# Performance work log

Measured on AMD Instinct MI355X. Metric: run time of the kernel, lower is better.

## Reference

```python
import jax, jax.numpy as jnp
import numpy as np

SEQ_LEN = 4096
EMBED_DIM = 1280
NUM_HEADS = 16
HEAD_DIM = EMBED_DIM // NUM_HEADS  # 80
SCALING = float(np.sqrt(HEAD_DIM))  # NOTE: source multiplies by sqrt(head_dim)
NEG_INF = float(np.finfo(np.float32).min)


def rotate_half(x):
    x1, x2 = jnp.split(x, 2, axis=-1)
    return jnp.concatenate((-x2, x1), axis=-1)


def setup_inputs() -> dict:
    key = jax.random.key(0)
    ks = jax.random.split(key, 7)
    s = 0.02
    hidden_states = jax.random.normal(ks[0], (SEQ_LEN, EMBED_DIM), dtype=jnp.float32)
    w_qkv = jax.random.normal(ks[1], (3 * EMBED_DIM, EMBED_DIM), dtype=jnp.float32) * s
    b_qkv = jax.random.normal(ks[2], (3 * EMBED_DIM,), dtype=jnp.float32) * s
    w_proj = jax.random.normal(ks[3], (EMBED_DIM, EMBED_DIM), dtype=jnp.float32) * s
    b_proj = jax.random.normal(ks[4], (EMBED_DIM,), dtype=jnp.float32) * s
    # rotary angles: theta duplicated to head_dim (emb = cat(rope, rope))
    inv_freq = 1.0 / (10000.0 ** (jnp.arange(0, HEAD_DIM // 2, dtype=jnp.float32) * 2.0 / HEAD_DIM))
    pos = jnp.arange(SEQ_LEN, dtype=jnp.float32)
    freqs = pos[:, None] * inv_freq[None, :]            # [S, hd/2]
    emb = jnp.concatenate((freqs, freqs), axis=-1)       # [S, hd]
    cos = jnp.cos(emb)
    sin = jnp.sin(emb)
    # 4 packed images of 1024 patches each
    cu_seqlens = jnp.array([0, 1024, 2048, 3072, 4096], dtype=jnp.int32)
    return {
        "hidden_states": hidden_states,
        "w_qkv": w_qkv, "b_qkv": b_qkv,
        "w_proj": w_proj, "b_proj": b_proj,
        "cos": cos, "sin": sin,
        "cu_seqlens": cu_seqlens,
    }


def reference(hidden_states, w_qkv, b_qkv, w_proj, b_proj, cos, sin, cu_seqlens):
    S = hidden_states.shape[0]
    # packed QKV projection
    qkv = hidden_states @ w_qkv.T + b_qkv                  # [S, 3D]
    qkv = qkv.reshape(S, 3, NUM_HEADS, HEAD_DIM)
    q, k, v = qkv[:, 0], qkv[:, 1], qkv[:, 2]              # [S, H, hd]
    # fp32 RoPE (broadcast cos/sin over heads)
    c = cos[:, None, :].astype(jnp.float32)
    sn = sin[:, None, :].astype(jnp.float32)
    qf, kf = q.astype(jnp.float32), k.astype(jnp.float32)
    q = (qf * c + rotate_half(qf) * sn).astype(q.dtype)
    k = (kf * c + rotate_half(kf) * sn).astype(k.dtype)
    # block-diagonal mask from cu_seqlens: same segment -> 0, else -inf
    pos = jnp.arange(S)
    seg = jnp.searchsorted(cu_seqlens, pos, side="right") - 1  # [S]
    bias = jnp.where(seg[:, None] == seg[None, :], 0.0, NEG_INF)  # [S, S]
    # dense attention over whole packed sequence (as in source)
    scores = jnp.einsum("shd,thd->hst", q, k) * SCALING + bias[None]
    weights = jax.nn.softmax(scores.astype(jnp.float32), axis=-1).astype(q.dtype)
    attn = jnp.einsum("hst,thd->shd", weights, v).reshape(S, EMBED_DIM)
    return attn @ w_proj.T + b_proj
```

## Files before the change

kernel.cpp:

```cpp
#include <hip/hip_runtime.h>

#define SEQ   4096
#define EMB   1280
#define NH    16
#define HD    80
#define HDP   96
#define O3    3840
#define SEGLEN 1024
#define NSEG  4
#define QSCALE (8.94427190999915878564f * 1.44269504088896340736f)

typedef unsigned short u16;
typedef __attribute__((ext_vector_type(8))) _Float16 f16x8;
typedef __attribute__((ext_vector_type(4))) _Float16 f16x4;
typedef __attribute__((ext_vector_type(2))) __fp16   h16x2;
typedef __attribute__((ext_vector_type(4))) float    f32x4;

__device__ __forceinline__ float ex2(float x) { return __builtin_amdgcn_exp2f(x); }

__device__ __forceinline__ u16 f2h(float f) {
  union { _Float16 h; u16 u; } v; v.h = (_Float16)f; return v.u;
}
__device__ __forceinline__ float h2f(u16 b) {
  union { u16 u; _Float16 h; } v; v.u = b; return (float)v.h;
}
__device__ __forceinline__ f32x4 exp2_4(f32x4 x) {
  f32x4 r; r.x = ex2(x.x); r.y = ex2(x.y); r.z = ex2(x.z); r.w = ex2(x.w); return r;
}
__device__ __forceinline__ f16x4 pk4(f32x4 s) {
  union { h16x2 h[2]; f16x4 f; } u;
  u.h[0] = __builtin_amdgcn_cvt_pkrtz(s.x, s.y);
  u.h[1] = __builtin_amdgcn_cvt_pkrtz(s.z, s.w);
  return u.f;
}
__device__ __forceinline__ void gl2lds16(const u16* g, u16* l) {
  __builtin_amdgcn_global_load_lds(
      (const __attribute__((address_space(1))) unsigned int*)g,
      (__attribute__((address_space(3))) unsigned int*)l, 16, 0, 0);
}

#define CVT_N1 (SEQ * EMB / 4)
#define CVT_N2 (O3 * EMB / 4)
#define CVT_N3 (EMB * EMB / 4)
__global__ void cvt_all_kernel(const float* __restrict__ a, const float* __restrict__ b,
                               const float* __restrict__ c, u16* __restrict__ oa,
                               u16* __restrict__ ob, u16* __restrict__ oc) {
  int i = blockIdx.x * blockDim.x + threadIdx.x;
  const float* src; u16* dst; int j = i;
  if (j < CVT_N1)                { src = a; dst = oa; }
  else if (j < CVT_N1 + CVT_N2)  { src = b; dst = ob; j -= CVT_N1; }
  else                           { src = c; dst = oc; j -= CVT_N1 + CVT_N2; }
  float4 f = ((const float4*)src)[j];
  union { u16 h[4]; uint2 v; } o;
  o.h[0] = f2h(f.x); o.h[1] = f2h(f.y); o.h[2] = f2h(f.z); o.h[3] = f2h(f.w);
  ((uint2*)dst)[j] = o.v;
}

template<int OUTF>
__global__ __launch_bounds__(256)
void gemm_bias_kernel(const u16* __restrict__ A, const u16* __restrict__ W,
                      const float* __restrict__ bias, void* __restrict__ Cout,
                      int N, int K) {
  __shared__ u16 As[128][64];
  __shared__ u16 Bs[128][64];
  const int tid  = threadIdx.x;
  const int flat = blockIdx.x + gridDim.x * blockIdx.y;
  const int cpx  = (gridDim.x * gridDim.y) >> 3;
  const int nid  = (flat & 7) * cpx + (flat >> 3);
  const int bm   = nid / gridDim.x, bn = nid % gridDim.x;
  const int lane = tid & 63;
  const int wid  = tid >> 6;
  const int wm   = (wid >> 1) * 64, wn = (wid & 1) * 64;
  const int lr   = lane & 15, quad = lane >> 4;

  f32x4 acc[4][4];
  const f32x4 z4 = {0.f, 0.f, 0.f, 0.f};
  #pragma unroll
  for (int i = 0; i < 4; ++i)
    #pragma unroll
    for (int j = 0; j < 4; ++j) acc[i][j] = z4;

  const int arow = tid >> 3;
  const int acol = (((tid & 7) ^ (arow & 7)) * 8);
  const u16* Ab = A + (size_t)(bm * 128) * K;
  const u16* Wb = W + (size_t)(bn * 128) * K;
  u16* AsL = &As[0][0] + tid * 8;
  u16* BsL = &Bs[0][0] + tid * 8;

  for (int kt = 0; kt < K; kt += 64) {
    #pragma unroll
    for (int r = 0; r < 4; ++r) {
      gl2lds16(&Ab[(size_t)(arow + r * 32) * K + kt + acol], AsL + r * 2048);
      gl2lds16(&Wb[(size_t)(arow + r * 32) * K + kt + acol], BsL + r * 2048);
    }
    __syncthreads();
    #pragma unroll
    for (int k32 = 0; k32 < 2; ++k32) {
      const int c = (((k32 * 4 + quad) ^ (lr & 7)) * 8);
      f16x8 aF[4], bF[4];
      #pragma unroll
      for (int i = 0; i < 4; ++i) {
        aF[i] = *(const f16x8*)&As[wm + i * 16 + lr][c];
        bF[i] = *(const f16x8*)&Bs[wn + i * 16 + lr][c];
      }
      #pragma unroll
      for (int i = 0; i < 4; ++i)
        #pragma unroll
        for (int j = 0; j < 4; ++j)
          acc[i][j] = __builtin_amdgcn_mfma_f32_16x16x32_f16(aF[i], bF[j], acc[i][j], 0, 0, 0);
    }
    __syncthreads();
  }

  #pragma unroll
  for (int i = 0; i < 4; ++i) {
    int rowb = bm * 128 + wm + i * 16 + quad * 4;
    #pragma unroll
    for (int j = 0; j < 4; ++j) {
      int col = bn * 128 + wn + j * 16 + lr;
      float bv = bias[col];
      #pragma unroll
      for (int r = 0; r < 4; ++r) {
        float v = acc[i][j][r] + bv;
        if (OUTF) ((float*)Cout)[(size_t)(rowb + r) * N + col] = v;
        else      ((u16*)Cout)[(size_t)(rowb + r) * N + col] = f2h(v);
      }
    }
  }
}

__global__ __launch_bounds__(512, 2)
void gemm256_kernel(const u16* __restrict__ A, const u16* __restrict__ W,
                    const float* __restrict__ bias, u16* __restrict__ Cout,
                    int N, int K) {
  __shared__ u16 As[2][256][64];
  __shared__ u16 Bs[2][256][64];
  const int tid  = threadIdx.x;
  const int flat = blockIdx.x + gridDim.x * blockIdx.y;
  const int cpx  = (gridDim.x * gridDim.y) >> 3;
  const int nid  = (flat & 7) * cpx + (flat >> 3);
  const int bm   = nid / gridDim.x, bn = nid % gridDim.x;
  const int lane = tid & 63;
  const int wid  = tid >> 6;
  const int wm   = wid >> 2;
  const int wn   = wid & 3;
  const int lr   = lane & 15, quad = lane >> 4;
  const int NT   = K >> 6;

  const u16* Ab = A + (size_t)(bm * 256) * K;
  const u16* Wb = W + (size_t)(bn * 256) * K;

  const int srr  = tid >> 3;
  const int scol = ((tid & 7) ^ (srr & 7)) << 3;
  const u16* ApL = Ab + (size_t)srr * K + scol;
  const u16* WpL = Wb + (size_t)srr * K + scol;

  auto stA = [&](int b, int row0, int t) {
    gl2lds16(ApL + (size_t)row0 * K + t * 64,        &As[b][row0][0]      + tid * 8);
    gl2lds16(ApL + (size_t)(row0 + 64) * K + t * 64, &As[b][row0 + 64][0] + tid * 8);
  };
  auto stB = [&](int b, int row0, int t) {
    gl2lds16(WpL + (size_t)row0 * K + t * 64,        &Bs[b][row0][0]      + tid * 8);
    gl2lds16(WpL + (size_t)(row0 + 64) * K + t * 64, &Bs[b][row0 + 64][0] + tid * 8);
  };

  f32x4 acc[8][4];
  const f32x4 z4 = {0.f, 0.f, 0.f, 0.f};
  #pragma unroll
  for (int i = 0; i < 8; ++i)
    #pragma unroll
    for (int j = 0; j < 4; ++j) acc[i][j] = z4;

  const int c0 = (((0 * 4 + quad) ^ (lr & 7)) << 3);
  const int c1 = (((1 * 4 + quad) ^ (lr & 7)) << 3);

  stA(0, 0, 0); stA(0, 128, 0);
  stB(0, 0, 0); stB(0, 128, 0);
  stA(1, 0, 1);
  asm volatile("s_waitcnt vmcnt(2)" ::: "memory");
  __builtin_amdgcn_s_barrier();
  __builtin_amdgcn_sched_barrier(0);

  for (int t = 0; t < NT; ++t) {
    const int buf = t & 1, nb = buf ^ 1;

    f16x8 bF[2][4], aF0[2][4];
    #pragma unroll
    for (int j = 0; j < 4; ++j) {
      bF[0][j] = *(const f16x8*)&Bs[buf][wn * 64 + j * 16 + lr][c0];
      bF[1][j] = *(const f16x8*)&Bs[buf][wn * 64 + j * 16 + lr][c1];
    }
    #pragma unroll
    for (int i = 0; i < 4; ++i) {
      aF0[0][i] = *(const f16x8*)&As[buf][wm * 64 + i * 16 + lr][c0];
      aF0[1][i] = *(const f16x8*)&As[buf][wm * 64 + i * 16 + lr][c1];
    }
    __builtin_amdgcn_sched_barrier(0);
    if (t + 1 < NT) { stB(nb, 0, t + 1); stB(nb, 128, t + 1); stA(nb, 128, t + 1); }
    __builtin_amdgcn_sched_barrier(0);
    __builtin_amdgcn_s_setprio(1);
    #pragma unroll
    for (int k32 = 0; k32 < 2; ++k32)
      #pragma unroll
      for (int i = 0; i < 4; ++i)
        #pragma unroll
        for (int j = 0; j < 4; ++j)
          acc[i][j] = __builtin_amdgcn_mfma_f32_16x16x32_f16(aF0[k32][i], bF[k32][j], acc[i][j], 0, 0, 0);
    __builtin_amdgcn_s_setprio(0);
    __builtin_amdgcn_sched_barrier(0);
    __builtin_amdgcn_s_barrier();

    f16x8 aF1[2][4];
    #pragma unroll
    for (int i = 0; i < 4; ++i) {
      aF1[0][i] = *(const f16x8*)&As[buf][128 + wm * 64 + i * 16 + lr][c0];
      aF1[1][i] = *(const f16x8*)&As[buf][128 + wm * 64 + i * 16 + lr][c1];
    }
    __builtin_amdgcn_sched_barrier(0);
    if (t + 2 < NT) stA(buf, 0, t + 2);
    __builtin_amdgcn_sched_barrier(0);
    __builtin_amdgcn_s_setprio(1);
    #pragma unroll
    for (int k32 = 0; k32 < 2; ++k32)
      #pragma unroll
      for (int i = 0; i < 4; ++i)
        #pragma unroll
        for (int j = 0; j < 4; ++j)
          acc[4 + i][j] = __builtin_amdgcn_mfma_f32_16x16x32_f16(aF1[k32][i], bF[k32][j], acc[4 + i][j], 0, 0, 0);
    __builtin_amdgcn_s_setprio(0);
    if (t < NT - 2) asm volatile("s_waitcnt vmcnt(2)" ::: "memory");
    else            asm volatile("s_waitcnt vmcnt(0)" ::: "memory");
    __builtin_amdgcn_s_barrier();
    __builtin_amdgcn_sched_barrier(0);
  }

  #pragma unroll
  for (int mq = 0; mq < 2; ++mq) {
    #pragma unroll
    for (int i = 0; i < 4; ++i) {
      const int rowb = bm * 256 + mq * 128 + wm * 64 + i * 16 + quad * 4;
      #pragma unroll
      for (int j = 0; j < 4; ++j) {
        const int col = bn * 256 + wn * 64 + j * 16 + lr;
        const float bv = bias[col];
        #pragma unroll
        for (int r = 0; r < 4; ++r)
          Cout[(size_t)(rowb + r) * N + col] = f2h(acc[mq * 4 + i][j][r] + bv);
      }
    }
  }
}

__global__ __launch_bounds__(256)
void rope_reorg_kernel(const u16* __restrict__ qkv, const float* __restrict__ cosp,
                       const float* __restrict__ sinp, u16* __restrict__ Qp,
                       u16* __restrict__ Kp, u16* __restrict__ Vt) {
  __shared__ u16 Qs[64][80];
  __shared__ u16 Ks[64][80];
  __shared__ u16 Vs[64][88];
  const int tid = threadIdx.x;
  const int s0 = blockIdx.x * 64;
  const int h  = blockIdx.y;

  for (int t = tid; t < 640; t += 256) {
    int r = t / 10, c = (t % 10) * 8;
    size_t g = (size_t)(s0 + r) * O3 + h * HD + c;
    *(uint4*)&Qs[r][c] = *(const uint4*)&qkv[g];
    *(uint4*)&Ks[r][c] = *(const uint4*)&qkv[g + EMB];
    *(uint4*)&Vs[r][c] = *(const uint4*)&qkv[g + 2 * EMB];
  }
  __syncthreads();

  for (int t = tid; t < 64 * 24; t += 256) {
    int r = t / 24, d4 = (t % 24) * 4;
    int s = s0 + r;
    size_t po = ((size_t)h * SEQ + s) * HDP + d4;
    if (d4 >= HD) {
      uint2 z = make_uint2(0, 0);
      *(uint2*)&Qp[po] = z; *(uint2*)&Kp[po] = z;
      continue;
    }
    float4 cv = *(const float4*)&cosp[(size_t)s * HD + d4];
    float4 sv = *(const float4*)&sinp[(size_t)s * HD + d4];
    int dp4 = (d4 < 40) ? d4 + 40 : d4 - 40;
    float sgn = (d4 < 40) ? -1.f : 1.f;
    union { u16 h[4]; uint2 v; } oq, ok;
    const float* cp = (const float*)&cv;
    const float* sp = (const float*)&sv;
    #pragma unroll
    for (int j = 0; j < 4; ++j) {
      float q  = h2f(Qs[r][d4 + j]),  k  = h2f(Ks[r][d4 + j]);
      float qp = h2f(Qs[r][dp4 + j]), kp = h2f(Ks[r][dp4 + j]);
      oq.h[j] = f2h((q * cp[j] + sgn * qp * sp[j]) * QSCALE);
      ok.h[j] = f2h(k * cp[j] + sgn * kp * sp[j]);
    }
    *(uint2*)&Qp[po] = oq.v;
    *(uint2*)&Kp[po] = ok.v;
  }

  for (int t = tid; t < HD * 8; t += 256) {
    int d = t / 8, sc = (t % 8) * 8;
    union { u16 h[8]; uint4 v; } o;
    #pragma unroll
    for (int j = 0; j < 8; ++j) o.h[j] = Vs[sc + j][d];
    *(uint4*)&Vt[((size_t)(h * HD + d)) * SEQ + s0 + sc] = o.v;
  }
}

__global__ __launch_bounds__(512)
void attn_kernel(const u16* __restrict__ Qp, const u16* __restrict__ Kp,
                 const u16* __restrict__ Vt, u16* __restrict__ attnO) {
  __shared__ u16 K_l[3][64][96];
  __shared__ u16 V_l[3][96][64];
  const int BUFSZ = 6144;
  const int NT = SEGLEN / 64;

  const int tid = threadIdx.x;
  const int lane = tid & 63, w = tid >> 6;
  const int lr = lane & 15, quad = lane >> 4;
  const int flat = blockIdx.x + 8 * blockIdx.y + 128 * blockIdx.z;
  const int nid  = (flat & 7) * 64 + (flat >> 3);
  const int qb   = nid & 7;
  const int h    = (nid >> 3) & 15;
  const int sg   = nid >> 7;
  const int seg0 = sg * SEGLEN;
  const int q0b = seg0 + qb * 128;

  f16x8 qF[3];
  {
    int qrow = q0b + w * 16 + lr;
    #pragma unroll
    for (int kc = 0; kc < 3; ++kc)
      qF[kc] = *(const f16x8*)&Qp[((size_t)h * SEQ + qrow) * HDP + kc * 32 + quad * 8];
  }
  asm volatile("" :: "v"(qF[0]), "v"(qF[1]), "v"(qF[2]));
  asm volatile("s_waitcnt vmcnt(0)" ::: "memory");

  {
    u16 val = (tid < 32) ? (u16)0x3C00 : (u16)0;
    #pragma unroll
    for (int b = 0; b < 3; ++b) {
      u16* q = &V_l[0][0][0] + b * BUFSZ + 80 * 64 + tid * 2;
      q[0] = val; q[1] = val;
    }
  }

  const u16* Kbase = Kp + ((size_t)h * SEQ + seg0) * HDP;
  const u16* Vbase = Vt + (size_t)h * HD * SEQ + seg0;
  const u16* pG[3]; u16* dB[3]; int gAdv[3];
  #pragma unroll
  for (int t = 0; t < 3; ++t) {
    int s = t * 512 + tid;
    if (s < 768) {
      int r = s / 12, c = s % 12;
      int ck = (c & ~3) | ((c & 3) ^ ((r >> 1) & 3));
      pG[t] = Kbase + (size_t)r * HDP + ck * 8;
      dB[t] = &K_l[0][0][0] + s * 8;
      gAdv[t] = 64 * HDP;
    } else {
      int sv = (s < 1408) ? s - 768 : s - 1408;
      int rv = sv / 8, cv = sv % 8;
      int cg = cv ^ (rv & 7);
      pG[t] = Vbase + (size_t)rv * SEQ + cg * 8;
      dB[t] = &V_l[0][0][0] + sv * 8;
      gAdv[t] = 64;
    }
  }

  auto stage_adv = [&](int b) {
    #pragma unroll
    for (int t = 0; t < 3; ++t) {
      gl2lds16(pG[t], dB[t] + b * BUFSZ);
      pG[t] += gAdv[t];
    }
  };

  const f32x4 z4 = {0.f, 0.f, 0.f, 0.f};
  float m_r = -3.0e38f;
  f32x4 Oacc[6];
  #pragma unroll
  for (int n = 0; n < 6; ++n) Oacc[n] = z4;

  const int kswz = (lr >> 1) & 3;

  auto qk = [&](f32x4 (&S)[4], const u16* kb) {
    __builtin_amdgcn_s_setprio(1);
    #pragma unroll
    for (int ct = 0; ct < 4; ++ct) {
      S[ct] = z4;
      #pragma unroll
      for (int kc = 0; kc < 3; ++kc) {
        f16x8 kF = *(const f16x8*)&kb[(ct * 16 + lr) * 96 + kc * 32 + ((quad ^ kswz) << 3)];
        S[ct] = __builtin_amdgcn_mfma_f32_16x16x32_f16(kF, qF[kc], S[ct], 0, 0, 0);
      }
    }
    __builtin_amdgcn_s_setprio(0);
  };

  auto smpv = [&](f32x4 (&S)[4], const u16* vb) {
    float mx = fmaxf(fmaxf(S[0].x, S[0].y), fmaxf(S[0].z, S[0].w));
    #pragma unroll
    for (int ct = 1; ct < 4; ++ct)
      mx = fmaxf(mx, fmaxf(fmaxf(S[ct].x, S[ct].y), fmaxf(S[ct].z, S[ct].w)));
    mx = fmaxf(mx, __shfl_xor(mx, 16, 64));
    mx = fmaxf(mx, __shfl_xor(mx, 32, 64));
    float mnew = fmaxf(m_r, mx);
    float alpha = ex2(m_r - mnew);
    m_r = mnew;

    f32x4 mv = {mnew, mnew, mnew, mnew};
    #pragma unroll
    for (int ct = 0; ct < 4; ++ct) S[ct] = exp2_4(S[ct] - mv);

    if (__ballot(alpha != 1.0f)) {
      f32x4 al;
      al.x = __shfl(alpha, quad * 4 + 0, 64);
      al.y = __shfl(alpha, quad * 4 + 1, 64);
      al.z = __shfl(alpha, quad * 4 + 2, 64);
      al.w = __shfl(alpha, quad * 4 + 3, 64);
      #pragma unroll
      for (int n = 0; n < 6; ++n) Oacc[n] *= al;
    }

    f16x4 pF[4];
    #pragma unroll
    for (int ct = 0; ct < 4; ++ct) pF[ct] = pk4(S[ct]);

    __builtin_amdgcn_s_setprio(1);
    #pragma unroll
    for (int ct = 0; ct < 4; ++ct) {
      const int cchunk = 2 * ct + (quad >> 1);
      #pragma unroll
      for (int n = 0; n < 6; ++n) {
        int vrow = n * 16 + lr;
        const u16* vp = vb + vrow * 64 + ((cchunk ^ (vrow & 7)) << 3) + ((quad & 1) << 2);
        f16x4 vF = *(const f16x4*)vp;
        Oacc[n] = __builtin_amdgcn_mfma_f32_16x16x16f16(pF[ct], vF, Oacc[n], 0, 0, 0);
      }
    }
    __builtin_amdgcn_s_setprio(0);
  };

  stage_adv(0);
  stage_adv(1);
  asm volatile("s_waitcnt vmcnt(3) lgkmcnt(0)" ::: "memory");
  __builtin_amdgcn_s_barrier();
  __builtin_amdgcn_sched_barrier(0);

  f32x4 Sa[4], Sb[4];
  qk(Sa, &K_l[0][0][0]);

  int buf = 0, sb = 2;
  auto iter = [&](int t, f32x4 (&Scur)[4], f32x4 (&Snext)[4]) {
    if (t + 2 < NT) {
      stage_adv(sb);
      asm volatile("s_waitcnt vmcnt(3)" ::: "memory");
    } else {
      asm volatile("s_waitcnt vmcnt(0)" ::: "memory");
    }
    __builtin_amdgcn_s_barrier();
    const int nbuf = (buf == 2) ? 0 : buf + 1;
    if (t + 1 < NT) qk(Snext, &K_l[0][0][0] + nbuf * BUFSZ);
    smpv(Scur, &V_l[0][0][0] + buf * BUFSZ);
    __builtin_amdgcn_sched_barrier(0);
    __builtin_amdgcn_s_barrier();
    buf = nbuf;
    sb = (sb == 2) ? 0 : sb + 1;
  };
  for (int tt = 0; tt < NT; tt += 2) {
    iter(tt, Sa, Sb);
    iter(tt + 1, Sb, Sa);
  }

  f32x4 linv;
  linv.x = 1.0f / __shfl(Oacc[5].x, quad << 4, 64);
  linv.y = 1.0f / __shfl(Oacc[5].y, quad << 4, 64);
  linv.z = 1.0f / __shfl(Oacc[5].z, quad << 4, 64);
  linv.w = 1.0f / __shfl(Oacc[5].w, quad << 4, 64);
  #pragma unroll
  for (int n = 0; n < 5; ++n) {
    int rowb = q0b + w * 16 + quad * 4;
    int col = h * HD + n * 16 + lr;
    attnO[(size_t)(rowb + 0) * EMB + col] = f2h(Oacc[n].x * linv.x);
    attnO[(size_t)(rowb + 1) * EMB + col] = f2h(Oacc[n].y * linv.y);
    attnO[(size_t)(rowb + 2) * EMB + col] = f2h(Oacc[n].z * linv.z);
    attnO[(size_t)(rowb + 3) * EMB + col] = f2h(Oacc[n].w * linv.w);
  }
}

extern "C" void kernel_launch(void* const* d_in, const int* in_sizes, int n_in,
                              void* d_out, int out_size, void* d_ws, size_t ws_size,
                              hipStream_t stream) {
  const float* hs     = (const float*)d_in[0];
  const float* w_qkv  = (const float*)d_in[1];
  const float* b_qkv  = (const float*)d_in[2];
  const float* w_proj = (const float*)d_in[3];
  const float* b_proj = (const float*)d_in[4];
  const float* cosp   = (const float*)d_in[5];
  const float* sinp   = (const float*)d_in[6];
  float* out = (float*)d_out;

  char* p = (char*)d_ws;
  auto take = [&](size_t bytes) { char* q = p; p += (bytes + 255) & ~(size_t)255; return q; };
  u16* hsH    = (u16*)take((size_t)SEQ * EMB * 2);
  u16* wqkvH  = (u16*)take((size_t)O3 * EMB * 2);
  u16* wprojH = (u16*)take((size_t)EMB * EMB * 2);
  u16* qkvO   = (u16*)take((size_t)SEQ * O3 * 2);
  u16* Qp     = (u16*)take((size_t)NH * SEQ * HDP * 2);
  u16* Kp     = (u16*)take((size_t)NH * SEQ * HDP * 2);
  u16* Vt     = (u16*)take((size_t)NH * HD * SEQ * 2);
  u16* attnH  = (u16*)take((size_t)SEQ * EMB * 2);

  int ncvt = (CVT_N1 + CVT_N2 + CVT_N3) / 256;
  cvt_all_kernel<<<ncvt, 256, 0, stream>>>(hs, w_qkv, w_proj, hsH, wqkvH, wprojH);

  gemm256_kernel<<<dim3(O3 / 256, SEQ / 256), 512, 0, stream>>>(hsH, wqkvH, b_qkv, qkvO, O3, EMB);

  rope_reorg_kernel<<<dim3(SEQ / 64, NH), 256, 0, stream>>>(qkvO, cosp, sinp, Qp, Kp, Vt);

  attn_kernel<<<dim3(SEGLEN / 128, NH, NSEG), 512, 0, stream>>>(Qp, Kp, Vt, attnH);

  gemm_bias_kernel<1><<<dim3(EMB / 128, SEQ / 128), 256, 0, stream>>>(attnH, wprojH, b_proj, out, EMB, EMB);
}
```

Baseline: 230.2 us.

## Process two 16-row query tiles per wave in attention with 256-thread blocks

The attention kernel now runs 4 waves per block instead of 8, and each wave handles 32 query rows as two 16-row tiles. Each K and V fragment read from LDS is reused for two MFMAs, which halves LDS read traffic per unit of work. The global-to-LDS staging is spread over 256 threads with twice as many loads each, and the wait counts are adjusted to match. The cost is roughly double the accumulator and score registers per wave and fewer waves per block to hide latency, which may lower occupancy.

```diff
diff --git a/kernel.cpp b/kernel.cpp
--- a/kernel.cpp
+++ b/kernel.cpp
@@ -307,7 +307,7 @@
   }
 }
 
-__global__ __launch_bounds__(512)
+__global__ __launch_bounds__(256)
 void attn_kernel(const u16* __restrict__ Qp, const u16* __restrict__ Kp,
                  const u16* __restrict__ Vt, u16* __restrict__ attnO) {
   __shared__ u16 K_l[3][64][96];
@@ -326,31 +326,33 @@
   const int seg0 = sg * SEGLEN;
   const int q0b = seg0 + qb * 128;
 
-  f16x8 qF[3];
+  f16x8 qF[2][3];
+  #pragma unroll
+  for (int qh = 0; qh < 2; ++qh) {
+    int qrow = q0b + w * 32 + qh * 16 + lr;
+    #pragma unroll
+    for (int kc = 0; kc < 3; ++kc)
+      qF[qh][kc] = *(const f16x8*)&Qp[((size_t)h * SEQ + qrow) * HDP + kc * 32 + quad * 8];
+  }
+  asm volatile("" :: "v"(qF[0][0]), "v"(qF[0][1]), "v"(qF[0][2]),
+                     "v"(qF[1][0]), "v"(qF[1][1]), "v"(qF[1][2]));
+  asm volatile("s_waitcnt vmcnt(0)" ::: "memory");
+
   {
-    int qrow = q0b + w * 16 + lr;
-    #pragma unroll
-    for (int kc = 0; kc < 3; ++kc)
-      qF[kc] = *(const f16x8*)&Qp[((size_t)h * SEQ + qrow) * HDP + kc * 32 + quad * 8];
-  }
-  asm volatile("" :: "v"(qF[0]), "v"(qF[1]), "v"(qF[2]));
-  asm volatile("s_waitcnt vmcnt(0)" ::: "memory");
-
-  {
-    u16 val = (tid < 32) ? (u16)0x3C00 : (u16)0;
+    u16 val = (tid < 16) ? (u16)0x3C00 : (u16)0;
     #pragma unroll
     for (int b = 0; b < 3; ++b) {
-      u16* q = &V_l[0][0][0] + b * BUFSZ + 80 * 64 + tid * 2;
-      q[0] = val; q[1] = val;
+      u16* q = &V_l[0][0][0] + b * BUFSZ + 80 * 64 + tid * 4;
+      q[0] = val; q[1] = val; q[2] = val; q[3] = val;
     }
   }
 
   const u16* Kbase = Kp + ((size_t)h * SEQ + seg0) * HDP;
   const u16* Vbase = Vt + (size_t)h * HD * SEQ + seg0;
-  const u16* pG[3]; u16* dB[3]; int gAdv[3];
-  #pragma unroll
-  for (int t = 0; t < 3; ++t) {
-    int s = t * 512 + tid;
+  const u16* pG[6]; u16* dB[6]; int gAdv[6];
+  #pragma unroll
+  for (int t = 0; t < 6; ++t) {
+    int s = t * 256 + tid;
     if (s < 768) {
       int r = s / 12, c = s % 12;
       int ck = (c & ~3) | ((c & 3) ^ ((r >> 1) & 3));
@@ -369,35 +371,36 @@
 
   auto stage_adv = [&](int b) {
     #pragma unroll
-    for (int t = 0; t < 3; ++t) {
+    for (int t = 0; t < 6; ++t) {
       gl2lds16(pG[t], dB[t] + b * BUFSZ);
       pG[t] += gAdv[t];
     }
   };
 
   const f32x4 z4 = {0.f, 0.f, 0.f, 0.f};
-  float m_r = -3.0e38f;
-  f32x4 Oacc[6];
-  #pragma unroll
-  for (int n = 0; n < 6; ++n) Oacc[n] = z4;
+  float m_r0 = -3.0e38f, m_r1 = -3.0e38f;
+  f32x4 Oacc0[6], Oacc1[6];
+  #pragma unroll
+  for (int n = 0; n < 6; ++n) { Oacc0[n] = z4; Oacc1[n] = z4; }
 
   const int kswz = (lr >> 1) & 3;
 
-  auto qk = [&](f32x4 (&S)[4], const u16* kb) {
+  auto qk = [&](f32x4 (&S)[2][4], const u16* kb) {
     __builtin_amdgcn_s_setprio(1);
     #pragma unroll
     for (int ct = 0; ct < 4; ++ct) {
-      S[ct] = z4;
+      S[0][ct] = z4; S[1][ct] = z4;
       #pragma unroll
       for (int kc = 0; kc < 3; ++kc) {
         f16x8 kF = *(const f16x8*)&kb[(ct * 16 + lr) * 96 + kc * 32 + ((quad ^ kswz) << 3)];
-        S[ct] = __builtin_amdgcn_mfma_f32_16x16x32_f16(kF, qF[kc], S[ct], 0, 0, 0);
+        S[0][ct] = __builtin_amdgcn_mfma_f32_16x16x32_f16(kF, qF[0][kc], S[0][ct], 0, 0, 0);
+        S[1][ct] = __builtin_amdgcn_mfma_f32_16x16x32_f16(kF, qF[1][kc], S[1][ct], 0, 0, 0);
       }
     }
     __builtin_amdgcn_s_setprio(0);
   };
 
-  auto smpv = [&](f32x4 (&S)[4], const u16* vb) {
+  auto smhalf = [&](f32x4 (&S)[4], f32x4 (&O)[6], float& m_r, f16x4 (&pF)[4]) {
     float mx = fmaxf(fmaxf(S[0].x, S[0].y), fmaxf(S[0].z, S[0].w));
     #pragma unroll
     for (int ct = 1; ct < 4; ++ct)
@@ -419,12 +422,17 @@
       al.z = __shfl(alpha, quad * 4 + 2, 64);
       al.w = __shfl(alpha, quad * 4 + 3, 64);
       #pragma unroll
-      for (int n = 0; n < 6; ++n) Oacc[n] *= al;
-    }
-
-    f16x4 pF[4];
+      for (int n = 0; n < 6; ++n) O[n] *= al;
+    }
+
     #pragma unroll
     for (int ct = 0; ct < 4; ++ct) pF[ct] = pk4(S[ct]);
+  };
+
+  auto smpv = [&](f32x4 (&S)[2][4], const u16* vb) {
+    f16x4 pF0[4], pF1[4];
+    smhalf(S[0], Oacc0, m_r0, pF0);
+    smhalf(S[1], Oacc1, m_r1, pF1);
 
     __builtin_amdgcn_s_setprio(1);
     #pragma unroll
@@ -435,7 +443,8 @@
         int vrow = n * 16 + lr;
         const u16* vp = vb + vrow * 64 + ((cchunk ^ (vrow & 7)) << 3) + ((quad & 1) << 2);
         f16x4 vF = *(const f16x4*)vp;
-        Oacc[n] = __builtin_amdgcn_mfma_f32_16x16x16f16(pF[ct], vF, Oacc[n], 0, 0, 0);
+        Oacc0[n] = __builtin_amdgcn_mfma_f32_16x16x16f16(pF0[ct], vF, Oacc0[n], 0, 0, 0);
+        Oacc1[n] = __builtin_amdgcn_mfma_f32_16x16x16f16(pF1[ct], vF, Oacc1[n], 0, 0, 0);
       }
     }
     __builtin_amdgcn_s_setprio(0);
@@ -443,18 +452,18 @@
 
   stage_adv(0);
   stage_adv(1);
-  asm volatile("s_waitcnt vmcnt(3) lgkmcnt(0)" ::: "memory");
+  asm volatile("s_waitcnt vmcnt(6) lgkmcnt(0)" ::: "memory");
   __builtin_amdgcn_s_barrier();
   __builtin_amdgcn_sched_barrier(0);
 
-  f32x4 Sa[4], Sb[4];
+  f32x4 Sa[2][4], Sb[2][4];
   qk(Sa, &K_l[0][0][0]);
 
   int buf = 0, sb = 2;
-  auto iter = [&](int t, f32x4 (&Scur)[4], f32x4 (&Snext)[4]) {
+  auto iter = [&](int t, f32x4 (&Scur)[2][4], f32x4 (&Snext)[2][4]) {
     if (t + 2 < NT) {
       stage_adv(sb);
-      asm volatile("s_waitcnt vmcnt(3)" ::: "memory");
+      asm volatile("s_waitcnt vmcnt(6)" ::: "memory");
     } else {
       asm volatile("s_waitcnt vmcnt(0)" ::: "memory");
     }
@@ -472,20 +481,24 @@
     iter(tt + 1, Sb, Sa);
   }
 
-  f32x4 linv;
-  linv.x = 1.0f / __shfl(Oacc[5].x, quad << 4, 64);
-  linv.y = 1.0f / __shfl(Oacc[5].y, quad << 4, 64);
-  linv.z = 1.0f / __shfl(Oacc[5].z, quad << 4, 64);
-  linv.w = 1.0f / __shfl(Oacc[5].w, quad << 4, 64);
-  #pragma unroll
-  for (int n = 0; n < 5; ++n) {
-    int rowb = q0b + w * 16 + quad * 4;
-    int col = h * HD + n * 16 + lr;
-    attnO[(size_t)(rowb + 0) * EMB + col] = f2h(Oacc[n].x * linv.x);
-    attnO[(size_t)(rowb + 1) * EMB + col] = f2h(Oacc[n].y * linv.y);
-    attnO[(size_t)(rowb + 2) * EMB + col] = f2h(Oacc[n].z * linv.z);
-    attnO[(size_t)(rowb + 3) * EMB + col] = f2h(Oacc[n].w * linv.w);
-  }
+  auto epi = [&](f32x4 (&O)[6], int qh) {
+    f32x4 linv;
+    linv.x = 1.0f / __shfl(O[5].x, quad << 4, 64);
+    linv.y = 1.0f / __shfl(O[5].y, quad << 4, 64);
+    linv.z = 1.0f / __shfl(O[5].z, quad << 4, 64);
+    linv.w = 1.0f / __shfl(O[5].w, quad << 4, 64);
+    #pragma unroll
+    for (int n = 0; n < 5; ++n) {
+      int rowb = q0b + w * 32 + qh * 16 + quad * 4;
+      int col = h * HD + n * 16 + lr;
+      attnO[(size_t)(rowb + 0) * EMB + col] = f2h(O[n].x * linv.x);
+      attnO[(size_t)(rowb + 1) * EMB + col] = f2h(O[n].y * linv.y);
+      attnO[(size_t)(rowb + 2) * EMB + col] = f2h(O[n].z * linv.z);
+      attnO[(size_t)(rowb + 3) * EMB + col] = f2h(O[n].w * linv.w);
+    }
+  };
+  epi(Oacc0, 0);
+  epi(Oacc1, 1);
 }
 
 extern "C" void kernel_launch(void* const* d_in, const int* in_sizes, int n_in,
@@ -518,7 +531,7 @@
 
   rope_reorg_kernel<<<dim3(SEQ / 64, NH), 256, 0, stream>>>(qkvO, cosp, sinp, Qp, Kp, Vt);
 
-  attn_kernel<<<dim3(SEGLEN / 128, NH, NSEG), 512, 0, stream>>>(Qp, Kp, Vt, attnH);
+  attn_kernel<<<dim3(SEGLEN / 128, NH, NSEG), 256, 0, stream>>>(Qp, Kp, Vt, attnH);
 
   gemm_bias_kernel<1><<<dim3(EMB / 128, SEQ / 128), 256, 0, stream>>>(attnH, wprojH, b_proj, out, EMB, EMB);
 }
```

Result: slower. 257.5 us (+11.9%).

## Double-buffer output projection GEMM with staged async loads and interleaved MFMA

Applied to the files above, without the earlier changes.

Replaces the simple single-buffered output projection GEMM with a double-buffered 128x128 kernel. Global-to-LDS loads for the next K tile are issued in two halves while MFMAs on the current tile run, using explicit vmcnt waits, raw barriers and priority hints. The wave layout also changes so each wave owns a 32-column strip across all 128 rows. The intent is to hide global load latency behind compute in a GEMM that is a modest share of total time. The cost is more LDS per block and fragile hand-written synchronisation.

```diff
diff --git a/kernel.cpp b/kernel.cpp
--- a/kernel.cpp
+++ b/kernel.cpp
@@ -56,13 +56,12 @@
   ((uint2*)dst)[j] = o.v;
 }
 
-template<int OUTF>
-__global__ __launch_bounds__(256)
-void gemm_bias_kernel(const u16* __restrict__ A, const u16* __restrict__ W,
-                      const float* __restrict__ bias, void* __restrict__ Cout,
-                      int N, int K) {
-  __shared__ u16 As[128][64];
-  __shared__ u16 Bs[128][64];
+__global__ __launch_bounds__(256, 2)
+void gemm128_kernel(const u16* __restrict__ A, const u16* __restrict__ W,
+                    const float* __restrict__ bias, float* __restrict__ Cout,
+                    int N, int K) {
+  __shared__ u16 As[2][128][64];
+  __shared__ u16 Bs[2][128][64];
   const int tid  = threadIdx.x;
   const int flat = blockIdx.x + gridDim.x * blockIdx.y;
   const int cpx  = (gridDim.x * gridDim.y) >> 3;
@@ -70,60 +69,106 @@
   const int bm   = nid / gridDim.x, bn = nid % gridDim.x;
   const int lane = tid & 63;
   const int wid  = tid >> 6;
-  const int wm   = (wid >> 1) * 64, wn = (wid & 1) * 64;
   const int lr   = lane & 15, quad = lane >> 4;
-
-  f32x4 acc[4][4];
-  const f32x4 z4 = {0.f, 0.f, 0.f, 0.f};
-  #pragma unroll
-  for (int i = 0; i < 4; ++i)
-    #pragma unroll
-    for (int j = 0; j < 4; ++j) acc[i][j] = z4;
-
-  const int arow = tid >> 3;
-  const int acol = (((tid & 7) ^ (arow & 7)) * 8);
+  const int NT   = K >> 6;
+
   const u16* Ab = A + (size_t)(bm * 128) * K;
   const u16* Wb = W + (size_t)(bn * 128) * K;
-  u16* AsL = &As[0][0] + tid * 8;
-  u16* BsL = &Bs[0][0] + tid * 8;
-
-  for (int kt = 0; kt < K; kt += 64) {
-    #pragma unroll
-    for (int r = 0; r < 4; ++r) {
-      gl2lds16(&Ab[(size_t)(arow + r * 32) * K + kt + acol], AsL + r * 2048);
-      gl2lds16(&Wb[(size_t)(arow + r * 32) * K + kt + acol], BsL + r * 2048);
-    }
-    __syncthreads();
-    #pragma unroll
-    for (int k32 = 0; k32 < 2; ++k32) {
-      const int c = (((k32 * 4 + quad) ^ (lr & 7)) * 8);
-      f16x8 aF[4], bF[4];
-      #pragma unroll
-      for (int i = 0; i < 4; ++i) {
-        aF[i] = *(const f16x8*)&As[wm + i * 16 + lr][c];
-        bF[i] = *(const f16x8*)&Bs[wn + i * 16 + lr][c];
-      }
+
+  const int arow = tid >> 3;
+  const int acol = ((tid & 7) ^ (arow & 7)) << 3;
+  const u16* ApL = Ab + (size_t)arow * K + acol;
+  const u16* WpL = Wb + (size_t)arow * K + acol;
+
+  auto stA = [&](int b, int row0, int t) {
+    gl2lds16(ApL + (size_t)row0 * K + t * 64,        &As[b][row0][0]      + tid * 8);
+    gl2lds16(ApL + (size_t)(row0 + 32) * K + t * 64, &As[b][row0 + 32][0] + tid * 8);
+  };
+  auto stB = [&](int b, int row0, int t) {
+    gl2lds16(WpL + (size_t)row0 * K + t * 64,        &Bs[b][row0][0]      + tid * 8);
+    gl2lds16(WpL + (size_t)(row0 + 32) * K + t * 64, &Bs[b][row0 + 32][0] + tid * 8);
+  };
+
+  f32x4 acc[8][2];
+  const f32x4 z4 = {0.f, 0.f, 0.f, 0.f};
+  #pragma unroll
+  for (int i = 0; i < 8; ++i) { acc[i][0] = z4; acc[i][1] = z4; }
+
+  const int c0 = (((0 * 4 + quad) ^ (lr & 7)) << 3);
+  const int c1 = (((1 * 4 + quad) ^ (lr & 7)) << 3);
+
+  stA(0, 0, 0); stA(0, 64, 0);
+  stB(0, 0, 0); stB(0, 64, 0);
+  stA(1, 0, 1);
+  asm volatile("s_waitcnt vmcnt(2)" ::: "memory");
+  __builtin_amdgcn_s_barrier();
+  __builtin_amdgcn_sched_barrier(0);
+
+  for (int t = 0; t < NT; ++t) {
+    const int buf = t & 1, nb = buf ^ 1;
+
+    f16x8 bF[2][2], aF0[2][4];
+    #pragma unroll
+    for (int j = 0; j < 2; ++j) {
+      bF[0][j] = *(const f16x8*)&Bs[buf][wid * 32 + j * 16 + lr][c0];
+      bF[1][j] = *(const f16x8*)&Bs[buf][wid * 32 + j * 16 + lr][c1];
+    }
+    #pragma unroll
+    for (int i = 0; i < 4; ++i) {
+      aF0[0][i] = *(const f16x8*)&As[buf][i * 16 + lr][c0];
+      aF0[1][i] = *(const f16x8*)&As[buf][i * 16 + lr][c1];
+    }
+    __builtin_amdgcn_sched_barrier(0);
+    if (t + 1 < NT) { stB(nb, 0, t + 1); stB(nb, 64, t + 1); stA(nb, 64, t + 1); }
+    __builtin_amdgcn_sched_barrier(0);
+    __builtin_amdgcn_s_setprio(1);
+    #pragma unroll
+    for (int k32 = 0; k32 < 2; ++k32)
       #pragma unroll
       for (int i = 0; i < 4; ++i)
         #pragma unroll
-        for (int j = 0; j < 4; ++j)
-          acc[i][j] = __builtin_amdgcn_mfma_f32_16x16x32_f16(aF[i], bF[j], acc[i][j], 0, 0, 0);
-    }
-    __syncthreads();
-  }
-
-  #pragma unroll
-  for (int i = 0; i < 4; ++i) {
-    int rowb = bm * 128 + wm + i * 16 + quad * 4;
-    #pragma unroll
-    for (int j = 0; j < 4; ++j) {
-      int col = bn * 128 + wn + j * 16 + lr;
-      float bv = bias[col];
-      #pragma unroll
-      for (int r = 0; r < 4; ++r) {
-        float v = acc[i][j][r] + bv;
-        if (OUTF) ((float*)Cout)[(size_t)(rowb + r) * N + col] = v;
-        else      ((u16*)Cout)[(size_t)(rowb + r) * N + col] = f2h(v);
+        for (int j = 0; j < 2; ++j)
+          acc[i][j] = __builtin_amdgcn_mfma_f32_16x16x32_f16(aF0[k32][i], bF[k32][j], acc[i][j], 0, 0, 0);
+    __builtin_amdgcn_s_setprio(0);
+    __builtin_amdgcn_sched_barrier(0);
+    __builtin_amdgcn_s_barrier();
+
+    f16x8 aF1[2][4];
+    #pragma unroll
+    for (int i = 0; i < 4; ++i) {
+      aF1[0][i] = *(const f16x8*)&As[buf][64 + i * 16 + lr][c0];
+      aF1[1][i] = *(const f16x8*)&As[buf][64 + i * 16 + lr][c1];
+    }
+    __builtin_amdgcn_sched_barrier(0);
+    if (t + 2 < NT) stA(buf, 0, t + 2);
+    __builtin_amdgcn_sched_barrier(0);
+    __builtin_amdgcn_s_setprio(1);
+    #pragma unroll
+    for (int k32 = 0; k32 < 2; ++k32)
+      #pragma unroll
+      for (int i = 0; i < 4; ++i)
+        #pragma unroll
+        for (int j = 0; j < 2; ++j)
+          acc[4 + i][j] = __builtin_amdgcn_mfma_f32_16x16x32_f16(aF1[k32][i], bF[k32][j], acc[4 + i][j], 0, 0, 0);
+    __builtin_amdgcn_s_setprio(0);
+    if (t < NT - 2) asm volatile("s_waitcnt vmcnt(2)" ::: "memory");
+    else            asm volatile("s_waitcnt vmcnt(0)" ::: "memory");
+    __builtin_amdgcn_s_barrier();
+    __builtin_amdgcn_sched_barrier(0);
+  }
+
+  #pragma unroll
+  for (int mq = 0; mq < 2; ++mq) {
+    #pragma unroll
+    for (int i = 0; i < 4; ++i) {
+      const int rowb = bm * 128 + mq * 64 + i * 16 + quad * 4;
+      #pragma unroll
+      for (int j = 0; j < 2; ++j) {
+        const int col = bn * 128 + wid * 32 + j * 16 + lr;
+        const float bv = bias[col];
+        #pragma unroll
+        for (int r = 0; r < 4; ++r)
+          Cout[(size_t)(rowb + r) * N + col] = acc[mq * 4 + i][j][r] + bv;
       }
     }
   }
@@ -520,5 +565,5 @@
 
   attn_kernel<<<dim3(SEGLEN / 128, NH, NSEG), 512, 0, stream>>>(Qp, Kp, Vt, attnH);
 
-  gemm_bias_kernel<1><<<dim3(EMB / 128, SEQ / 128), 256, 0, stream>>>(attnH, wprojH, b_proj, out, EMB, EMB);
-}
+  gemm128_kernel<<<dim3(EMB / 128, SEQ / 128), 256, 0, stream>>>(attnH, wprojH, b_proj, out, EMB, EMB);
+}
```

Measured after the change: 221.2 us. -3.9%, faster.
